# Optimization experiments

Measured on AMD Instinct MI355X. Metric: run time of the kernel, lower is better.

The kernel has to match this reference:

```python
import jax, jax.numpy as jnp
import numpy as np

D_MODEL = 1024
HEADS = 16
D_FF = 4096
EPS = 1e-6
NEG = -1e9


def setup_inputs() -> dict:
    key = jax.random.key(0)
    ks = jax.random.split(key, 12)
    B, S, D = 2, 2048, D_MODEL
    s = 0.02
    return {
        "x": jax.random.normal(ks[0], (B, S, D), dtype=jnp.float32),
        "mask": jax.random.randint(ks[1], (B, 1, S), 0, 2, dtype=jnp.int32),
        "alpha1": jnp.ones((D,), jnp.float32),
        "bias1": jnp.zeros((D,), jnp.float32),
        "alpha2": jnp.ones((D,), jnp.float32),
        "bias2": jnp.zeros((D,), jnp.float32),
        "Wk": jax.random.normal(ks[2], (D, D), jnp.float32) * s,
        "bk": jnp.zeros((D,), jnp.float32),
        "Wv": jax.random.normal(ks[3], (D, D), jnp.float32) * s,
        "bv": jnp.zeros((D,), jnp.float32),
        "Wo": jax.random.normal(ks[4], (D, D), jnp.float32) * s,
        "bo": jnp.zeros((D,), jnp.float32),
        "W1": jax.random.normal(ks[5], (D, D_FF), jnp.float32) * s,
        "b1": jnp.zeros((D_FF,), jnp.float32),
        "W2": jax.random.normal(ks[6], (D_FF, D), jnp.float32) * s,
        "b2": jnp.zeros((D,), jnp.float32),
    }


def _norm(x, alpha, bias):
    # torch Norm: unbiased std (ddof=1), eps added to std (not variance)
    mu = jnp.mean(x, axis=-1, keepdims=True)
    sd = jnp.std(x, axis=-1, keepdims=True, ddof=1)
    return alpha * (x - mu) / (sd + EPS) + bias


def reference(x, mask, alpha1, bias1, alpha2, bias2,
              Wk, bk, Wv, bv, Wo, bo, W1, b1, W2, b2):
    B, S, D = x.shape
    H, dk = HEADS, D // HEADS

    x2 = _norm(x, alpha1, bias1)
    # NOTE: source bug preserved: q uses k_linear weights
    q = (x2 @ Wk + bk).reshape(B, S, H, dk).transpose(0, 2, 1, 3)  # [B,H,S,dk]
    k = (x2 @ Wk + bk).reshape(B, S, H, dk).transpose(0, 2, 1, 3)
    v = (x2 @ Wv + bv).reshape(B, S, H, dk).transpose(0, 2, 1, 3)

    scores = jnp.einsum('bhqd,bhkd->bhqk', q, k) / jnp.sqrt(jnp.float32(dk))
    scores = jnp.where(mask[:, None, :, :] == 0, NEG, scores)  # [B,1,1,S] broadcast
    attn = jax.nn.softmax(scores, axis=-1)
    ctx = jnp.einsum('bhqk,bhkd->bhqd', attn, v)
    concat = ctx.transpose(0, 2, 1, 3).reshape(B, S, D)
    x = x + (concat @ Wo + bo)

    x2 = _norm(x, alpha2, bias2)
    ff = jax.nn.relu(x2 @ W1 + b1) @ W2 + b2
    return x + ff
```

## Files before the change

### kernel.cpp

```cpp
#include <hip/hip_runtime.h>
#include <hip/hip_bf16.h>
#include <math.h>

typedef __bf16 bf16_t;
typedef __bf16 bf16x8 __attribute__((ext_vector_type(8)));
typedef __bf16 bf16x4 __attribute__((ext_vector_type(4)));
typedef float  f32x4  __attribute__((ext_vector_type(4)));

#define MFMA16(a,b,c) __builtin_amdgcn_mfma_f32_16x16x32_bf16((a),(b),(c),0,0,0)

__device__ static inline void gload_lds16(const void* g, void* l) {
    __builtin_amdgcn_global_load_lds((const __attribute__((address_space(1))) void*)g,
                                     (__attribute__((address_space(3))) void*)l, 16, 0, 0);
}

__device__ static inline float exp2_hw(float x) {
#if __has_builtin(__builtin_amdgcn_exp2f)
    return __builtin_amdgcn_exp2f(x);
#else
    float r; asm("v_exp_f32 %0, %1" : "=v"(r) : "v"(x)); return r;
#endif
}

__global__ __launch_bounds__(256)
void preamble_k(const float* __restrict__ Wk, const float* __restrict__ Wv,
                const float* __restrict__ Wo, const float* __restrict__ W1,
                const float* __restrict__ W2,
                bf16_t* __restrict__ WkT, bf16_t* __restrict__ WvT,
                bf16_t* __restrict__ WoT, bf16_t* __restrict__ W1T,
                bf16_t* __restrict__ W2T,
                const float* __restrict__ bk, const float* __restrict__ bv,
                float* __restrict__ bkv,
                const int* __restrict__ msk, float* __restrict__ mbias)
{
    __shared__ float t[32][33];
    const int id = blockIdx.x;
    if (id < 11264) {
        const float* in; bf16_t* out; int R, C, bx, by;
        if (id < 3072) {
            R = 1024; C = 1024;
            const int wsel = id >> 10, lid = id & 1023;
            in  = (wsel == 0) ? Wk : (wsel == 1) ? Wv : Wo;
            out = (wsel == 0) ? WkT : (wsel == 1) ? WvT : WoT;
            bx = lid & 31; by = lid >> 5;
        } else if (id < 7168) {
            R = 1024; C = 4096; const int lid = id - 3072;
            in = W1; out = W1T;
            bx = lid & 127; by = lid >> 7;
        } else {
            R = 4096; C = 1024; const int lid = id - 7168;
            in = W2; out = W2T;
            bx = lid & 31; by = lid >> 5;
        }
        const int tx = threadIdx.x & 31, ty = threadIdx.x >> 5;
        const int r0 = by << 5, c0 = bx << 5;
#pragma unroll
        for (int i = 0; i < 4; ++i)
            t[ty + i*8][tx] = in[(size_t)(r0 + ty + i*8) * C + c0 + tx];
        __syncthreads();
#pragma unroll
        for (int i = 0; i < 4; ++i)
            out[(size_t)(c0 + ty + i*8) * R + r0 + tx] = (bf16_t)t[tx][ty + i*8];
    } else if (id < 11272) {
        const int i = (id - 11264) * 256 + threadIdx.x;
        bkv[i] = (i < 1024) ? bk[i] : bv[i - 1024];
    } else {
        const int i = (id - 11272) * 256 + threadIdx.x;
        mbias[i] = (msk[i] == 0) ? -16384.0f : -16.0f;
    }
}

__global__ __launch_bounds__(256)
void layernorm_k(const float* __restrict__ x, const float* __restrict__ gam,
                 const float* __restrict__ bet, bf16_t* __restrict__ out)
{
    const int row = blockIdx.x, tid = threadIdx.x;
    const float4 v = ((const float4*)(x + (size_t)row * 1024))[tid];
    float s  = v.x + v.y + v.z + v.w;
    float ss = v.x*v.x + v.y*v.y + v.z*v.z + v.w*v.w;
#pragma unroll
    for (int off = 32; off >= 1; off >>= 1) {
        s  += __shfl_xor(s,  off);
        ss += __shfl_xor(ss, off);
    }
    __shared__ float rs[4], rq[4];
    if ((tid & 63) == 0) { rs[tid >> 6] = s; rq[tid >> 6] = ss; }
    __syncthreads();
    s  = rs[0] + rs[1] + rs[2] + rs[3];
    ss = rq[0] + rq[1] + rq[2] + rq[3];
    const float mu  = s * (1.0f / 1024.0f);
    const float var = fmaxf((ss - 1024.0f * mu * mu) * (1.0f / 1023.0f), 0.0f);
    const float inv = 1.0f / (sqrtf(var) + 1e-6f);
    const int c = tid << 2;
    bf16x4 o;
    o[0] = (bf16_t)(gam[c+0] * ((v.x - mu) * inv) + bet[c+0]);
    o[1] = (bf16_t)(gam[c+1] * ((v.y - mu) * inv) + bet[c+1]);
    o[2] = (bf16_t)(gam[c+2] * ((v.z - mu) * inv) + bet[c+2]);
    o[3] = (bf16_t)(gam[c+3] * ((v.w - mu) * inv) + bet[c+3]);
    *(bf16x4*)(out + (size_t)row * 1024 + c) = o;
}

template<bool RELU, bool RES, int NFR, bool DBUF, bool VT>
__global__ __launch_bounds__(256, 2)
void gemm128(const bf16_t* __restrict__ A, const bf16_t* __restrict__ Bt,
             const float* __restrict__ bias, const float* __restrict__ res,
             bf16_t* __restrict__ Cb, float* __restrict__ Cf,
             bf16_t* __restrict__ Cv,
             int M, int N, int K)
{
    constexpr int NTILE = NFR * 32;
    constexpr int NBUF = DBUF ? 2 : 1;
    __shared__ __align__(16) bf16_t As[NBUF][128 * 64];
    __shared__ __align__(16) bf16_t Bs[NBUF][NTILE * 64];
    const int tid  = threadIdx.x;
    const int lane = tid & 63;
    const int wid  = tid >> 6;
    const int wr = wid >> 1, wc = wid & 1;
    const int ntn = N / NTILE;
    const int cpx = gridDim.x >> 3;
    const int swz = (blockIdx.x & 7) * cpx + (blockIdx.x >> 3);
    const int bm = (swz / ntn) << 7;
    const int bn = (swz % ntn) * NTILE;
    const int l15 = lane & 15;
    const int g   = lane >> 4;

    f32x4 acc[4][NFR];
#pragma unroll
    for (int i = 0; i < 4; ++i)
#pragma unroll
        for (int j = 0; j < NFR; ++j)
#pragma unroll
            for (int e = 0; e < 4; ++e) acc[i][j][e] = 0.0f;

    const int srow = tid >> 3;
    const int scb  = (((tid & 7) << 4) ^ ((srow & 7) << 4));
    const bf16_t* Ab = A  + (size_t)(bm + srow) * K + (scb >> 1);
    const bf16_t* Bb = Bt + (size_t)(bn + srow) * K + (scb >> 1);

    auto stage = [&](int buf, int kt) {
        const int k0 = kt << 6;
        bf16_t* AsB = As[buf] + wid * 512;
        bf16_t* BsB = Bs[buf] + wid * 512;
#pragma unroll
        for (int it = 0; it < 4; ++it)
            gload_lds16(Ab + k0 + (size_t)(it * 32) * K, AsB + it * 2048);
#pragma unroll
        for (int it = 0; it < NFR; ++it)
            gload_lds16(Bb + k0 + (size_t)(it * 32) * K, BsB + it * 2048);
    };

    auto compute = [&](int buf) {
        bf16x8 af[4][2], bfr[NFR][2];
#pragma unroll
        for (int mi = 0; mi < 4; ++mi) {
            const int ar = (wr << 6) + mi * 16 + l15;
#pragma unroll
            for (int ks = 0; ks < 2; ++ks) {
                const int kb = (ks << 6) + (g << 4);
                af[mi][ks] = *(const bf16x8*)((const char*)As[buf] + ar * 128 + (kb ^ ((ar & 7) << 4)));
            }
        }
#pragma unroll
        for (int ni = 0; ni < NFR; ++ni) {
            const int br = wc * (NFR * 16) + ni * 16 + l15;
#pragma unroll
            for (int ks = 0; ks < 2; ++ks) {
                const int kb = (ks << 6) + (g << 4);
                bfr[ni][ks] = *(const bf16x8*)((const char*)Bs[buf] + br * 128 + (kb ^ ((br & 7) << 4)));
            }
        }
#pragma unroll
        for (int mi = 0; mi < 4; ++mi)
#pragma unroll
            for (int ni = 0; ni < NFR; ++ni) {
                acc[mi][ni] = MFMA16(af[mi][0], bfr[ni][0], acc[mi][ni]);
                acc[mi][ni] = MFMA16(af[mi][1], bfr[ni][1], acc[mi][ni]);
            }
    };

    const int nK = K >> 6;
    if constexpr (DBUF) {
        stage(0, 0);
        __syncthreads();
        for (int kt = 0; kt < nK; ++kt) {
            const int cur = kt & 1;
            if (kt + 1 < nK) stage(cur ^ 1, kt + 1);
            compute(cur);
            __syncthreads();
        }
    } else {
        for (int kt = 0; kt < nK; ++kt) {
            stage(0, kt);
            __syncthreads();
            compute(0);
            __syncthreads();
        }
    }

    if (VT && bn >= 1024) {
#pragma unroll
        for (int mi = 0; mi < 4; ++mi)
#pragma unroll
            for (int ni = 0; ni < NFR; ++ni) {
                const int gc = bn - 1024 + wc * (NFR * 16) + ni * 16 + l15;
                const float bv = bias[gc + 1024];
                bf16x4 o;
#pragma unroll
                for (int j = 0; j < 4; ++j) o[j] = (bf16_t)(acc[mi][ni][j] + bv);
                *(bf16x4*)(Cv + (size_t)gc * 4096 + bm + (wr << 6) + mi * 16 + (g << 2)) = o;
            }
        return;
    }

#pragma unroll
    for (int mi = 0; mi < 4; ++mi)
#pragma unroll
        for (int ni = 0; ni < NFR; ++ni) {
            const int gc = bn + wc * (NFR * 16) + ni * 16 + l15;
            const float bv = bias[gc];
#pragma unroll
            for (int j = 0; j < 4; ++j) {
                const int gr = bm + (wr << 6) + mi * 16 + (g << 2) + j;
                float vv = acc[mi][ni][j] + bv;
                if (RELU) vv = fmaxf(vv, 0.0f);
                if (RES)  Cf[(size_t)gr * N + gc] = vv + res[(size_t)gr * N + gc];
                else      Cb[(size_t)gr * N + gc] = (bf16_t)vv;
            }
        }
}

template<bool RELU, bool RES, int NFR>
__global__ __launch_bounds__(256, 2)
void gemm_pipe3(const bf16_t* __restrict__ A, const bf16_t* __restrict__ Bt,
                const float* __restrict__ bias, const float* __restrict__ res,
                bf16_t* __restrict__ Cb, float* __restrict__ Cf,
                int M, int N, int K)
{
    constexpr int NTILE = NFR * 32;
    constexpr int LOADS = 4 + NFR;
    __shared__ __align__(16) bf16_t As[3][128 * 64];
    __shared__ __align__(16) bf16_t Bs[3][NTILE * 64];
    const int tid  = threadIdx.x;
    const int lane = tid & 63;
    const int wid  = tid >> 6;
    const int wr = wid >> 1, wc = wid & 1;
    const int ntn = N / NTILE;
    const int cpx = gridDim.x >> 3;
    const int swz = (blockIdx.x & 7) * cpx + (blockIdx.x >> 3);
    const int bm = (swz / ntn) << 7;
    const int bn = (swz % ntn) * NTILE;
    const int l15 = lane & 15;
    const int g   = lane >> 4;

    f32x4 acc[4][NFR];
#pragma unroll
    for (int i = 0; i < 4; ++i)
#pragma unroll
        for (int j = 0; j < NFR; ++j)
#pragma unroll
            for (int e = 0; e < 4; ++e) acc[i][j][e] = 0.0f;

    const int srow = tid >> 3;
    const int scb  = (((tid & 7) << 4) ^ ((srow & 7) << 4));
    const bf16_t* Ab = A  + (size_t)(bm + srow) * K + (scb >> 1);
    const bf16_t* Bb = Bt + (size_t)(bn + srow) * K + (scb >> 1);

    auto stage = [&](int buf, int kt) {
        const int k0 = kt << 6;
        bf16_t* AsB = As[buf] + wid * 512;
        bf16_t* BsB = Bs[buf] + wid * 512;
#pragma unroll
        for (int it = 0; it < 4; ++it)
            gload_lds16(Ab + k0 + (size_t)(it * 32) * K, AsB + it * 2048);
#pragma unroll
        for (int it = 0; it < NFR; ++it)
            gload_lds16(Bb + k0 + (size_t)(it * 32) * K, BsB + it * 2048);
    };

    auto compute = [&](int buf) {
        bf16x8 af[4][2], bfr[NFR][2];
#pragma unroll
        for (int mi = 0; mi < 4; ++mi) {
            const int ar = (wr << 6) + mi * 16 + l15;
#pragma unroll
            for (int ks = 0; ks < 2; ++ks) {
                const int kb = (ks << 6) + (g << 4);
                af[mi][ks] = *(const bf16x8*)((const char*)As[buf] + ar * 128 + (kb ^ ((ar & 7) << 4)));
            }
        }
#pragma unroll
        for (int ni = 0; ni < NFR; ++ni) {
            const int br = wc * (NFR * 16) + ni * 16 + l15;
#pragma unroll
            for (int ks = 0; ks < 2; ++ks) {
                const int kb = (ks << 6) + (g << 4);
                bfr[ni][ks] = *(const bf16x8*)((const char*)Bs[buf] + br * 128 + (kb ^ ((br & 7) << 4)));
            }
        }
#pragma unroll
        for (int mi = 0; mi < 4; ++mi)
#pragma unroll
            for (int ni = 0; ni < NFR; ++ni) {
                acc[mi][ni] = MFMA16(af[mi][0], bfr[ni][0], acc[mi][ni]);
                acc[mi][ni] = MFMA16(af[mi][1], bfr[ni][1], acc[mi][ni]);
            }
    };

    const int nK = K >> 6;
    stage(0, 0);
    stage(1, 1);
    for (int kt = 0; kt < nK; ++kt) {
        if (kt + 1 < nK) {
            asm volatile("s_waitcnt vmcnt(%0)" :: "i"(LOADS) : "memory");
        } else {
            asm volatile("s_waitcnt vmcnt(0)" ::: "memory");
        }
        __builtin_amdgcn_sched_barrier(0);
        __builtin_amdgcn_s_barrier();
        asm volatile("" ::: "memory");
        if (kt + 2 < nK) stage((kt + 2) % 3, kt + 2);
        compute(kt % 3);
    }

#pragma unroll
    for (int mi = 0; mi < 4; ++mi)
#pragma unroll
        for (int ni = 0; ni < NFR; ++ni) {
            const int gc = bn + wc * (NFR * 16) + ni * 16 + l15;
            const float bv = bias[gc];
#pragma unroll
            for (int j = 0; j < 4; ++j) {
                const int gr = bm + (wr << 6) + mi * 16 + (g << 2) + j;
                float vv = acc[mi][ni][j] + bv;
                if (RELU) vv = fmaxf(vv, 0.0f);
                if (RES)  Cf[(size_t)gr * N + gc] = vv + res[(size_t)gr * N + gc];
                else      Cb[(size_t)gr * N + gc] = (bf16_t)vv;
            }
        }
}

__global__ __launch_bounds__(256, 3)
void attn_kernel(const bf16_t* __restrict__ qkv, const bf16_t* __restrict__ vT,
                 const float* __restrict__ mbias, bf16_t* __restrict__ ctx)
{
    __shared__ __align__(16) bf16_t Ks[2][64 * 64];
    __shared__ __align__(16) bf16_t Vs[2][64 * 64];
    __shared__ __align__(16) char   Ps[4][4096];

    const int tid = threadIdx.x, lane = tid & 63, wid = tid >> 6;
    const int l15 = lane & 15, g = lane >> 4;
    const int id = blockIdx.x;
    const int qt = (id >> 3) & 15;
    const int bh = (id & 7) * 4 + (id >> 7);
    const int b = bh >> 4, h = bh & 15;
    const size_t rowQ = (size_t)(b * 2048 + qt * 128 + wid * 32);
    const float C = 0.18033688f;

    bf16x8 qf[2][2];
#pragma unroll
    for (int qfi = 0; qfi < 2; ++qfi)
#pragma unroll
        for (int ks = 0; ks < 2; ++ks)
            qf[qfi][ks] = *(const bf16x8*)(qkv + (rowQ + qfi*16 + l15) * 2048
                                           + h*64 + ks*32 + g*8);

    bf16x8 vones;
#pragma unroll
    for (int e = 0; e < 8; ++e) vones[e] = (bf16_t)1.0f;

    f32x4 O[2][4], l_acc[2];
#pragma unroll
    for (int mf = 0; mf < 2; ++mf) {
#pragma unroll
        for (int df = 0; df < 4; ++df)
#pragma unroll
            for (int e = 0; e < 4; ++e) O[mf][df][e] = 0.0f;
#pragma unroll
        for (int e = 0; e < 4; ++e) l_acc[mf][e] = 0.0f;
    }

    const int srow = tid >> 3;
    const int scb  = (((tid & 7) << 4) ^ ((srow & 7) << 4));
    const bf16_t* Kb = qkv + (size_t)(b*2048 + srow) * 2048 + h*64 + (scb >> 1);
    const bf16_t* Vb = vT  + (size_t)(h*64 + srow) * 4096 + b*2048 + (scb >> 1);
    const float*  Mb = mbias + b*2048;
    bf16_t* Ks0 = Ks[0] + wid * 512;  bf16_t* Ks1 = Ks[1] + wid * 512;
    bf16_t* Vs0 = Vs[0] + wid * 512;  bf16_t* Vs1 = Vs[1] + wid * 512;

    #define STAGE(KD, VD, KT)                                        \
        do {                                                         \
            gload_lds16(Kb + (size_t)(KT) * 2048, (KD));             \
            gload_lds16(Kb + (size_t)((KT) + 32) * 2048, (KD) + 2048);\
            gload_lds16(Vb + (KT), (VD));                            \
            gload_lds16(Vb + (size_t)32 * 4096 + (KT), (VD) + 2048); \
        } while (0)

    STAGE(Ks0, Vs0, 0);
    __syncthreads();

    char* Pw = Ps[wid];

    for (int kt_i = 0; kt_i < 32; ++kt_i) {
        const int kt = kt_i << 6;
        const bool cur1 = (kt_i & 1);
        if (kt_i < 31) {
            if (cur1) STAGE(Ks0, Vs0, kt + 64);
            else      STAGE(Ks1, Vs1, kt + 64);
        }
        const char* Kc = (const char*)(cur1 ? Ks[1] : Ks[0]);
        const char* Vc = (const char*)(cur1 ? Vs[1] : Vs[0]);

        bf16x8 kf[4][2];
#pragma unroll
        for (int kfi = 0; kfi < 4; ++kfi) {
            const int kr = kfi*16 + l15;
#pragma unroll
            for (int ks = 0; ks < 2; ++ks)
                kf[kfi][ks] = *(const bf16x8*)(Kc + kr*128
                                               + ((ks*64 + g*16) ^ ((kr & 7) << 4)));
        }
        f32x4 st[4][2];
#pragma unroll
        for (int kfi = 0; kfi < 4; ++kfi)
#pragma unroll
            for (int qfi = 0; qfi < 2; ++qfi) {
                f32x4 t;
#pragma unroll
                for (int e = 0; e < 4; ++e) t[e] = 0.0f;
                t = MFMA16(kf[kfi][0], qf[qfi][0], t);
                t = MFMA16(kf[kfi][1], qf[qfi][1], t);
                st[kfi][qfi] = t;
            }

        bf16x8 vf[4][2];
#pragma unroll
        for (int df = 0; df < 4; ++df) {
            const int vr = df*16 + l15;
#pragma unroll
            for (int ks = 0; ks < 2; ++ks)
                vf[df][ks] = *(const bf16x8*)(Vc + vr*128
                                              + ((ks*64 + g*16) ^ ((vr & 7) << 4)));
        }

#pragma unroll
        for (int kfi = 0; kfi < 4; ++kfi) {
            const float4 bb = *(const float4*)(Mb + kt + kfi*16 + g*4);
            const float* bj = (const float*)&bb;
#pragma unroll
            for (int qfi = 0; qfi < 2; ++qfi) {
                const int q = qfi*16 + l15;
                bf16x4 pk;
#pragma unroll
                for (int j = 0; j < 4; ++j)
                    pk[j] = (bf16_t)exp2_hw(fmaf(st[kfi][qfi][j], C, bj[j]));
                *(bf16x4*)(Pw + q*128 + ((kfi*32 + g*8) ^ ((l15 & 7) << 4))) = pk;
            }
        }
        bf16x8 pa[2][2];
#pragma unroll
        for (int mf = 0; mf < 2; ++mf) {
            const int r = mf*16 + l15;
#pragma unroll
            for (int ks = 0; ks < 2; ++ks)
                pa[mf][ks] = *(const bf16x8*)(Pw + r*128 + ((ks*64 + g*16) ^ ((l15 & 7) << 4)));
        }
#pragma unroll
        for (int mf = 0; mf < 2; ++mf) {
#pragma unroll
            for (int df = 0; df < 4; ++df) {
                O[mf][df] = MFMA16(pa[mf][0], vf[df][0], O[mf][df]);
                O[mf][df] = MFMA16(pa[mf][1], vf[df][1], O[mf][df]);
            }
            l_acc[mf] = MFMA16(pa[mf][0], vones, l_acc[mf]);
            l_acc[mf] = MFMA16(pa[mf][1], vones, l_acc[mf]);
        }
        __syncthreads();
    }
    #undef STAGE

#pragma unroll
    for (int mf = 0; mf < 2; ++mf)
#pragma unroll
        for (int j = 0; j < 4; ++j) {
            const float ri = __builtin_amdgcn_rcpf(l_acc[mf][j]);
            const size_t gr = rowQ + mf*16 + g*4 + j;
#pragma unroll
            for (int df = 0; df < 4; ++df)
                ctx[gr * 1024 + h*64 + df*16 + l15] = (bf16_t)(O[mf][df][j] * ri);
        }
}

extern "C" void kernel_launch(void* const* d_in, const int* in_sizes, int n_in,
                              void* d_out, int out_size, void* d_ws, size_t ws_size,
                              hipStream_t stream)
{
    const float* x   = (const float*)d_in[0];
    const int*   msk = (const int*)  d_in[1];
    const float* a1  = (const float*)d_in[2];
    const float* be1 = (const float*)d_in[3];
    const float* a2  = (const float*)d_in[4];
    const float* be2 = (const float*)d_in[5];
    const float* Wk  = (const float*)d_in[6];
    const float* bk  = (const float*)d_in[7];
    const float* Wv  = (const float*)d_in[8];
    const float* bv  = (const float*)d_in[9];
    const float* Wo  = (const float*)d_in[10];
    const float* bo  = (const float*)d_in[11];
    const float* W1  = (const float*)d_in[12];
    const float* b1  = (const float*)d_in[13];
    const float* W2  = (const float*)d_in[14];
    const float* b2  = (const float*)d_in[15];
    float* out = (float*)d_out;

    char* ws = (char*)d_ws;
    const size_t MB = 1u << 20;
    if (ws_size < 78 * MB) return;
    bf16_t* WkT = (bf16_t*)(ws + 0 * MB);
    bf16_t* WvT = (bf16_t*)(ws + 2 * MB);
    bf16_t* WoT = (bf16_t*)(ws + 4 * MB);
    bf16_t* W1T = (bf16_t*)(ws + 6 * MB);
    bf16_t* W2T = (bf16_t*)(ws + 14 * MB);
    bf16_t* x2  = (bf16_t*)(ws + 22 * MB);
    bf16_t* qkv = (bf16_t*)(ws + 30 * MB);
    bf16_t* vTb = (bf16_t*)(ws + 46 * MB);
    bf16_t* ctx = (bf16_t*)(ws + 54 * MB);
    float*  xn  = (float*) (ws + 62 * MB);
    float*  bkv   = (float*)(ws + 62 * MB);
    float*  mbias = (float*)(ws + 62 * MB + 32768);
    bf16_t* hb  = (bf16_t*)(ws + 30 * MB);

    dim3 blk(256);
    preamble_k<<<dim3(11288), blk, 0, stream>>>(Wk, Wv, Wo, W1, W2,
                                                WkT, WvT, WoT, W1T, W2T,
                                                bk, bv, bkv, msk, mbias);

    layernorm_k<<<4096, blk, 0, stream>>>(x, a1, be1, x2);
    gemm128<false,false,4,true,true><<<dim3(32 * 16), blk, 0, stream>>>(x2, WkT, bkv, nullptr, qkv, nullptr, vTb, 4096, 2048, 1024);
    attn_kernel<<<dim3(512), blk, 0, stream>>>(qkv, vTb, mbias, ctx);
    gemm_pipe3<false,true,2><<<dim3(32 * 16), blk, 0, stream>>>(ctx, WoT, bo, x,  nullptr, xn, 4096, 1024, 1024);
    layernorm_k<<<4096, blk, 0, stream>>>(xn, a2, be2, x2);
    gemm128<true,false,4,false,false><<<dim3(32 * 32), blk, 0, stream>>>(x2, W1T, b1, nullptr, hb, nullptr, nullptr, 4096, 4096, 1024);
    gemm_pipe3<false,true,2><<<dim3(32 * 16), blk, 0, stream>>>(hb, W2T, b2, xn, nullptr, out, 4096, 1024, 4096);
}
```

Before: 225.4 us.

## Replace 128x64 triple-buffered GEMM with 64x64 double-buffered tile for N=1024 GEMMs

The Wo and W2 projections (N=1024) now use a new 64x64 tile kernel with two-stage buffering and plain __syncthreads in place of the 128x64 three-stage pipeline with manual vmcnt waits. The grid doubles to 1024 blocks, meant to give better occupancy and CU fill on the narrow-N GEMMs. The cost is lower data reuse per block, meaning more global/L2 traffic per FLOP. The weaker pipelining may also expose load latency, especially in the K=4096 W2 GEMM.

Result: faster. 217.1 us (-3.7%).

```diff
diff --git a/kernel.cpp b/kernel.cpp
--- a/kernel.cpp
+++ b/kernel.cpp
@@ -229,34 +229,30 @@
         }
 }
 
-template<bool RELU, bool RES, int NFR>
-__global__ __launch_bounds__(256, 2)
-void gemm_pipe3(const bf16_t* __restrict__ A, const bf16_t* __restrict__ Bt,
-                const float* __restrict__ bias, const float* __restrict__ res,
-                bf16_t* __restrict__ Cb, float* __restrict__ Cf,
-                int M, int N, int K)
+__global__ __launch_bounds__(256, 4)
+void gemm64(const bf16_t* __restrict__ A, const bf16_t* __restrict__ Bt,
+            const float* __restrict__ bias, const float* __restrict__ res,
+            float* __restrict__ Cf, int M, int N, int K)
 {
-    constexpr int NTILE = NFR * 32;
-    constexpr int LOADS = 4 + NFR;
-    __shared__ __align__(16) bf16_t As[3][128 * 64];
-    __shared__ __align__(16) bf16_t Bs[3][NTILE * 64];
+    __shared__ __align__(16) bf16_t As[2][64 * 64];
+    __shared__ __align__(16) bf16_t Bs[2][64 * 64];
     const int tid  = threadIdx.x;
     const int lane = tid & 63;
     const int wid  = tid >> 6;
     const int wr = wid >> 1, wc = wid & 1;
-    const int ntn = N / NTILE;
+    const int ntn = N >> 6;
     const int cpx = gridDim.x >> 3;
     const int swz = (blockIdx.x & 7) * cpx + (blockIdx.x >> 3);
-    const int bm = (swz / ntn) << 7;
-    const int bn = (swz % ntn) * NTILE;
+    const int bm = (swz / ntn) << 6;
+    const int bn = (swz % ntn) << 6;
     const int l15 = lane & 15;
     const int g   = lane >> 4;
 
-    f32x4 acc[4][NFR];
-#pragma unroll
-    for (int i = 0; i < 4; ++i)
-#pragma unroll
-        for (int j = 0; j < NFR; ++j)
+    f32x4 acc[2][2];
+#pragma unroll
+    for (int i = 0; i < 2; ++i)
+#pragma unroll
+        for (int j = 0; j < 2; ++j)
 #pragma unroll
             for (int e = 0; e < 4; ++e) acc[i][j][e] = 0.0f;
 
@@ -270,18 +266,18 @@
         bf16_t* AsB = As[buf] + wid * 512;
         bf16_t* BsB = Bs[buf] + wid * 512;
 #pragma unroll
-        for (int it = 0; it < 4; ++it)
+        for (int it = 0; it < 2; ++it)
             gload_lds16(Ab + k0 + (size_t)(it * 32) * K, AsB + it * 2048);
 #pragma unroll
-        for (int it = 0; it < NFR; ++it)
+        for (int it = 0; it < 2; ++it)
             gload_lds16(Bb + k0 + (size_t)(it * 32) * K, BsB + it * 2048);
     };
 
     auto compute = [&](int buf) {
-        bf16x8 af[4][2], bfr[NFR][2];
-#pragma unroll
-        for (int mi = 0; mi < 4; ++mi) {
-            const int ar = (wr << 6) + mi * 16 + l15;
+        bf16x8 af[2][2], bfr[2][2];
+#pragma unroll
+        for (int mi = 0; mi < 2; ++mi) {
+            const int ar = (wr << 5) + mi * 16 + l15;
 #pragma unroll
             for (int ks = 0; ks < 2; ++ks) {
                 const int kb = (ks << 6) + (g << 4);
@@ -289,8 +285,8 @@
             }
         }
 #pragma unroll
-        for (int ni = 0; ni < NFR; ++ni) {
-            const int br = wc * (NFR * 16) + ni * 16 + l15;
+        for (int ni = 0; ni < 2; ++ni) {
+            const int br = (wc << 5) + ni * 16 + l15;
 #pragma unroll
             for (int ks = 0; ks < 2; ++ks) {
                 const int kb = (ks << 6) + (g << 4);
@@ -298,9 +294,9 @@
             }
         }
 #pragma unroll
-        for (int mi = 0; mi < 4; ++mi)
-#pragma unroll
-            for (int ni = 0; ni < NFR; ++ni) {
+        for (int mi = 0; mi < 2; ++mi)
+#pragma unroll
+            for (int ni = 0; ni < 2; ++ni) {
                 acc[mi][ni] = MFMA16(af[mi][0], bfr[ni][0], acc[mi][ni]);
                 acc[mi][ni] = MFMA16(af[mi][1], bfr[ni][1], acc[mi][ni]);
             }
@@ -308,33 +304,24 @@
 
     const int nK = K >> 6;
     stage(0, 0);
-    stage(1, 1);
+    __syncthreads();
     for (int kt = 0; kt < nK; ++kt) {
-        if (kt + 1 < nK) {
-            asm volatile("s_waitcnt vmcnt(%0)" :: "i"(LOADS) : "memory");
-        } else {
-            asm volatile("s_waitcnt vmcnt(0)" ::: "memory");
-        }
-        __builtin_amdgcn_sched_barrier(0);
-        __builtin_amdgcn_s_barrier();
-        asm volatile("" ::: "memory");
-        if (kt + 2 < nK) stage((kt + 2) % 3, kt + 2);
-        compute(kt % 3);
-    }
-
-#pragma unroll
-    for (int mi = 0; mi < 4; ++mi)
-#pragma unroll
-        for (int ni = 0; ni < NFR; ++ni) {
-            const int gc = bn + wc * (NFR * 16) + ni * 16 + l15;
+        const int cur = kt & 1;
+        if (kt + 1 < nK) stage(cur ^ 1, kt + 1);
+        compute(cur);
+        __syncthreads();
+    }
+
+#pragma unroll
+    for (int mi = 0; mi < 2; ++mi)
+#pragma unroll
+        for (int ni = 0; ni < 2; ++ni) {
+            const int gc = bn + (wc << 5) + ni * 16 + l15;
             const float bv = bias[gc];
 #pragma unroll
             for (int j = 0; j < 4; ++j) {
-                const int gr = bm + (wr << 6) + mi * 16 + (g << 2) + j;
-                float vv = acc[mi][ni][j] + bv;
-                if (RELU) vv = fmaxf(vv, 0.0f);
-                if (RES)  Cf[(size_t)gr * N + gc] = vv + res[(size_t)gr * N + gc];
-                else      Cb[(size_t)gr * N + gc] = (bf16_t)vv;
+                const int gr = bm + (wr << 5) + mi * 16 + (g << 2) + j;
+                Cf[(size_t)gr * N + gc] = acc[mi][ni][j] + bv + res[(size_t)gr * N + gc];
             }
         }
 }
@@ -537,8 +524,8 @@
     layernorm_k<<<4096, blk, 0, stream>>>(x, a1, be1, x2);
     gemm128<false,false,4,true,true><<<dim3(32 * 16), blk, 0, stream>>>(x2, WkT, bkv, nullptr, qkv, nullptr, vTb, 4096, 2048, 1024);
     attn_kernel<<<dim3(512), blk, 0, stream>>>(qkv, vTb, mbias, ctx);
-    gemm_pipe3<false,true,2><<<dim3(32 * 16), blk, 0, stream>>>(ctx, WoT, bo, x,  nullptr, xn, 4096, 1024, 1024);
+    gemm64<<<dim3(64 * 16), blk, 0, stream>>>(ctx, WoT, bo, x, xn, 4096, 1024, 1024);
     layernorm_k<<<4096, blk, 0, stream>>>(xn, a2, be2, x2);
     gemm128<true,false,4,false,false><<<dim3(32 * 32), blk, 0, stream>>>(x2, W1T, b1, nullptr, hb, nullptr, nullptr, 4096, 4096, 1024);
-    gemm_pipe3<false,true,2><<<dim3(32 * 16), blk, 0, stream>>>(hb, W2T, b2, xn, nullptr, out, 4096, 1024, 4096);
-}
+    gemm64<<<dim3(64 * 16), blk, 0, stream>>>(hb, W2T, b2, xn, out, 4096, 1024, 4096);
+}
```
